# Performance work log

Hardware: AMD Instinct MI355X
Metric: run time of the kernel (lower is better)

The kernel has to match this reference:

```python
import jax, jax.numpy as jnp
import numpy as np

B, N, A, IN_DIM, OUT_DIM, D_OBS = 4096, 16, 8, 128, 128, 128


def setup_inputs() -> dict:
    key = jax.random.key(0)
    k1, k2, k3, k4, k5, k6 = jax.random.split(key, 6)
    h = jax.random.normal(k1, (B, N, IN_DIM), dtype=jnp.float32)
    policies = jax.random.uniform(k2, (B, N, A), dtype=jnp.float32)
    actions = jax.random.uniform(k3, (B, N, A), dtype=jnp.float32)
    obs_proc = jax.random.normal(k4, (B * N, D_OBS), dtype=jnp.float32)
    # xavier-normal-ish params (exact init values irrelevant for correctness baseline)
    W_fc = jax.random.normal(k5, (OUT_DIM, IN_DIM), dtype=jnp.float32) * (2.0 / (IN_DIM + OUT_DIM)) ** 0.5
    W_attn = jax.random.normal(k6, (1, 2 * OUT_DIM), dtype=jnp.float32) * (2.0 / (2 * OUT_DIM + 1)) ** 0.5
    return {"h": h, "policies": policies, "actions": actions, "obs_proc": obs_proc,
            "W_fc": W_fc, "W_attn": W_attn}


def reference(h, policies, actions, obs_proc, W_fc, W_attn):
    # h: [B, N, in_dim]; policies/actions: [B, N, A]; obs_proc: [B*N, D]
    b, n, a = policies.shape
    z = jnp.einsum('bni,oi->bno', h, W_fc)                    # fc(h), [B, N, out]
    out_dim = z.shape[-1]
    # attn_fc(cat[z_src, z_dst]) split into src/dst contributions
    a_src = z @ W_attn[0, :out_dim]                           # [B, N]
    a_dst = z @ W_attn[0, out_dim:]                           # [B, N]
    # e[b, i(dst), j(src)] = leaky_relu(a_src[b,j] + a_dst[b,i])
    e = jax.nn.leaky_relu(a_src[:, None, :] + a_dst[:, :, None], 0.01)
    w = jax.nn.sigmoid(e)[..., None]                          # [B, N(dst), N(src), 1]
    # gated mix of source action / source policy per (dst, src) pair
    zgate = w * actions[:, None, :, :] + (1.0 - w) * policies[:, None, :, :]  # [B,i,j,A]
    # repeat + place_policies/place_zs masked sum + mean over src dim collapses to:
    # out_z[b,i,k] = (sum_j zgate[b,i,j] - zgate[b,i,k] + policies[b,k]) / N
    sum_z = zgate.sum(axis=2)                                 # [B, i, A]
    out_z = (sum_z[:, :, None, :] - zgate + policies[:, None, :, :]) / n  # [B,i,k,A]
    obs_b = obs_proc.reshape(b, n, -1)                        # [B, k, D]
    d = obs_b.shape[-1]
    obs_rep = jnp.broadcast_to(obs_b[:, None, :, :], (b, n, n, d))  # [B, i, k, D]
    obs_final = jnp.concatenate([obs_rep, out_z], axis=-1).reshape(b * n, n, d + a)
    return obs_final, w.reshape(b * n, n, 1)
```

## Files before the change

kernel.cpp:

```cpp
#include <hip/hip_runtime.h>
#include <math.h>

#define B_SZ 4096
#define N_SZ 16
#define A_SZ 8
#define IN_DIM 128
#define OUT_DIM 128
#define D_OBS 128
#define ROW_OUT (D_OBS + A_SZ)

typedef float f32x4 __attribute__((ext_vector_type(4)));

__global__ __launch_bounds__(256) void prep_v(const float* __restrict__ W_fc,
                                              const float* __restrict__ W_attn,
                                              float* __restrict__ v) {
  __shared__ float part[2][2][128];
  const int i = threadIdx.x & 127;
  const int half = threadIdx.x >> 7;
  float s = 0.f, d = 0.f;
  #pragma unroll 8
  for (int oo = 0; oo < 64; ++oo) {
    const int o = half * 64 + oo;
    const float w = W_fc[o * IN_DIM + i];
    s += w * W_attn[o];
    d += w * W_attn[OUT_DIM + o];
  }
  part[half][0][i] = s;
  part[half][1][i] = d;
  __syncthreads();
  if (half == 0) {
    v[i]          = part[0][0][i] + part[1][0][i];
    v[IN_DIM + i] = part[0][1][i] + part[1][1][i];
  }
}

__global__ __launch_bounds__(256) void gat_main(
    const float* __restrict__ h,
    const float* __restrict__ pol,
    const float* __restrict__ act,
    const float* __restrict__ obs,
    const float* __restrict__ v,
    float* __restrict__ out_obs,
    float* __restrict__ out_w)
{
  const int b = blockIdx.x;
  const int tid = threadIdx.x;

  __shared__ float a_src_sm[16];
  __shared__ float a_dst_sm[16];
  __shared__ float w_sm[256];
  __shared__ float pol_sm[128];
  __shared__ float act_sm[128];
  __shared__ float sumz_sm[128];
  __shared__ float outz_sm[2048];
  __shared__ float obs_sm[2048];

  {
    const f32x4* op = (const f32x4*)(obs + (size_t)b * (N_SZ * D_OBS));
    f32x4* od = (f32x4*)obs_sm;
    od[tid]       = __builtin_nontemporal_load(&op[tid]);
    od[tid + 256] = __builtin_nontemporal_load(&op[tid + 256]);
  }
  if (tid < 128) {
    pol_sm[tid] = __builtin_nontemporal_load(&pol[(size_t)b * (N_SZ * A_SZ) + tid]);
    act_sm[tid] = __builtin_nontemporal_load(&act[(size_t)b * (N_SZ * A_SZ) + tid]);
  }

  {
    const int n = tid >> 4;
    const int l = tid & 15;
    const f32x4* hp = (const f32x4*)(h + (size_t)b * (N_SZ * IN_DIM));
    const f32x4 h0 = __builtin_nontemporal_load(&hp[tid * 2]);
    const f32x4 h1 = __builtin_nontemporal_load(&hp[tid * 2 + 1]);
    const f32x4* vs = (const f32x4*)v;
    const f32x4* vd = (const f32x4*)(v + IN_DIM);
    const f32x4 s0 = vs[l * 2], s1 = vs[l * 2 + 1];
    const f32x4 d0 = vd[l * 2], d1 = vd[l * 2 + 1];
    float s = h0.x * s0.x + h0.y * s0.y + h0.z * s0.z + h0.w * s0.w
            + h1.x * s1.x + h1.y * s1.y + h1.z * s1.z + h1.w * s1.w;
    float d = h0.x * d0.x + h0.y * d0.y + h0.z * d0.z + h0.w * d0.w
            + h1.x * d1.x + h1.y * d1.y + h1.z * d1.z + h1.w * d1.w;
    for (int m = 8; m >= 1; m >>= 1) {
      s += __shfl_xor(s, m, 16);
      d += __shfl_xor(d, m, 16);
    }
    if (l == 0) {
      a_src_sm[n] = s;
      a_dst_sm[n] = d;
    }
  }
  __syncthreads();

  {
    const int i = tid >> 4, j = tid & 15;
    float e = a_src_sm[j] + a_dst_sm[i];
    e = (e >= 0.f) ? e : 0.01f * e;
    const float wv = 1.f / (1.f + expf(-e));
    w_sm[tid] = wv;
    __builtin_nontemporal_store(wv, &out_w[(size_t)b * 256 + tid]);
  }
  __syncthreads();

  if (tid < 128) {
    const int i = tid >> 3, a = tid & 7;
    float s = 0.f;
    for (int j = 0; j < N_SZ; ++j) {
      const float wv = w_sm[i * 16 + j];
      s += wv * act_sm[j * 8 + a] + (1.f - wv) * pol_sm[j * 8 + a];
    }
    sumz_sm[tid] = s;
  }
  __syncthreads();

  {
    const int i = tid >> 4, k = tid & 15;
    const float wv = w_sm[tid];
    for (int a = 0; a < A_SZ; ++a) {
      const float zg = wv * act_sm[k * 8 + a] + (1.f - wv) * pol_sm[k * 8 + a];
      outz_sm[tid * 8 + a] =
          (sumz_sm[i * 8 + a] - zg + pol_sm[k * 8 + a]) * 0.0625f;
    }
  }
  __syncthreads();

  float* ob = out_obs + (size_t)b * (256 * ROW_OUT);
  const f32x4* obs4 = (const f32x4*)obs_sm;
  #pragma unroll 2
  for (int idx = tid; idx < 256 * 34; idx += 256) {
    const int r = idx / 34;
    const int d4 = idx - r * 34;
    f32x4 o4;
    if (d4 < 32) {
      const int k = r & 15;
      o4 = obs4[k * 32 + d4];
    } else {
      o4 = *(const f32x4*)(outz_sm + r * 8 + (d4 - 32) * 4);
    }
    __builtin_nontemporal_store(o4, (f32x4*)(ob + (size_t)idx * 4));
  }
}

extern "C" void kernel_launch(void* const* d_in, const int* in_sizes, int n_in,
                              void* d_out, int out_size, void* d_ws, size_t ws_size,
                              hipStream_t stream) {
  const float* h      = (const float*)d_in[0];
  const float* pol    = (const float*)d_in[1];
  const float* act    = (const float*)d_in[2];
  const float* obs    = (const float*)d_in[3];
  const float* W_fc   = (const float*)d_in[4];
  const float* W_attn = (const float*)d_in[5];

  float* out = (float*)d_out;
  float* out_w = out + (size_t)B_SZ * N_SZ * N_SZ * ROW_OUT;
  float* v = (float*)d_ws;

  prep_v<<<1, 256, 0, stream>>>(W_fc, W_attn, v);
  gat_main<<<B_SZ, 256, 0, stream>>>(h, pol, act, obs, v, out, out_w);
}
```

Before: 138.8 us.

## Split obs broadcast into separate grid-stride streaming kernel, widen prep reduction

The monolithic per-batch kernel is split in two. One kernel computes the attention weights and writes the 8-float gate columns of each output row directly from registers. A separate grid-stride kernel copies the broadcast obs rows into the first 128 columns of each output row. The prep kernel also uses 1024 threads with 8 partial sums instead of 256. This removes the large shared-memory staging and per-block syncs, and the copy loop drops its branch. In exchange it adds a third launch and leaves two kernels writing interleaved parts of the same rows, so each row's 544-byte span is covered by two partial, strided writes.

```diff
diff --git a/kernel.cpp b/kernel.cpp
--- a/kernel.cpp
+++ b/kernel.cpp
@@ -11,34 +11,36 @@
 
 typedef float f32x4 __attribute__((ext_vector_type(4)));
 
-__global__ __launch_bounds__(256) void prep_v(const float* __restrict__ W_fc,
-                                              const float* __restrict__ W_attn,
-                                              float* __restrict__ v) {
-  __shared__ float part[2][2][128];
+__global__ __launch_bounds__(1024) void prep_v(const float* __restrict__ W_fc,
+                                               const float* __restrict__ W_attn,
+                                               float* __restrict__ v) {
+  __shared__ float part[8][2][128];
   const int i = threadIdx.x & 127;
-  const int half = threadIdx.x >> 7;
+  const int seg = threadIdx.x >> 7;
   float s = 0.f, d = 0.f;
-  #pragma unroll 8
-  for (int oo = 0; oo < 64; ++oo) {
-    const int o = half * 64 + oo;
+  #pragma unroll
+  for (int oo = 0; oo < 16; ++oo) {
+    const int o = seg * 16 + oo;
     const float w = W_fc[o * IN_DIM + i];
     s += w * W_attn[o];
     d += w * W_attn[OUT_DIM + o];
   }
-  part[half][0][i] = s;
-  part[half][1][i] = d;
+  part[seg][0][i] = s;
+  part[seg][1][i] = d;
   __syncthreads();
-  if (half == 0) {
-    v[i]          = part[0][0][i] + part[1][0][i];
-    v[IN_DIM + i] = part[0][1][i] + part[1][1][i];
+  if (seg == 0) {
+    float ss = 0.f, dd = 0.f;
+    #pragma unroll
+    for (int t = 0; t < 8; ++t) { ss += part[t][0][i]; dd += part[t][1][i]; }
+    v[i] = ss;
+    v[IN_DIM + i] = dd;
   }
 }
 
-__global__ __launch_bounds__(256) void gat_main(
+__global__ __launch_bounds__(256) void gat_compute(
     const float* __restrict__ h,
     const float* __restrict__ pol,
     const float* __restrict__ act,
-    const float* __restrict__ obs,
     const float* __restrict__ v,
     float* __restrict__ out_obs,
     float* __restrict__ out_w)
@@ -52,15 +54,7 @@
   __shared__ float pol_sm[128];
   __shared__ float act_sm[128];
   __shared__ float sumz_sm[128];
-  __shared__ float outz_sm[2048];
-  __shared__ float obs_sm[2048];
 
-  {
-    const f32x4* op = (const f32x4*)(obs + (size_t)b * (N_SZ * D_OBS));
-    f32x4* od = (f32x4*)obs_sm;
-    od[tid]       = __builtin_nontemporal_load(&op[tid]);
-    od[tid + 256] = __builtin_nontemporal_load(&op[tid + 256]);
-  }
   if (tid < 128) {
     pol_sm[tid] = __builtin_nontemporal_load(&pol[(size_t)b * (N_SZ * A_SZ) + tid]);
     act_sm[tid] = __builtin_nontemporal_load(&act[(size_t)b * (N_SZ * A_SZ) + tid]);
@@ -113,30 +107,37 @@
   __syncthreads();
 
   {
-    const int i = tid >> 4, k = tid & 15;
+    const int k = tid & 15;
     const float wv = w_sm[tid];
+    float o8[8];
+    #pragma unroll
     for (int a = 0; a < A_SZ; ++a) {
       const float zg = wv * act_sm[k * 8 + a] + (1.f - wv) * pol_sm[k * 8 + a];
-      outz_sm[tid * 8 + a] =
-          (sumz_sm[i * 8 + a] - zg + pol_sm[k * 8 + a]) * 0.0625f;
+      o8[a] = (sumz_sm[(tid >> 4) * 8 + a] - zg + pol_sm[k * 8 + a]) * 0.0625f;
     }
+    const size_t row = (size_t)b * 256 + tid;
+    f32x4* dst = (f32x4*)(out_obs + row * ROW_OUT + D_OBS);
+    f32x4 lo = {o8[0], o8[1], o8[2], o8[3]};
+    f32x4 hi = {o8[4], o8[5], o8[6], o8[7]};
+    __builtin_nontemporal_store(lo, dst);
+    __builtin_nontemporal_store(hi, dst + 1);
   }
-  __syncthreads();
+}
 
-  float* ob = out_obs + (size_t)b * (256 * ROW_OUT);
-  const f32x4* obs4 = (const f32x4*)obs_sm;
-  #pragma unroll 2
-  for (int idx = tid; idx < 256 * 34; idx += 256) {
-    const int r = idx / 34;
-    const int d4 = idx - r * 34;
-    f32x4 o4;
-    if (d4 < 32) {
-      const int k = r & 15;
-      o4 = obs4[k * 32 + d4];
-    } else {
-      o4 = *(const f32x4*)(outz_sm + r * 8 + (d4 - 32) * 4);
-    }
-    __builtin_nontemporal_store(o4, (f32x4*)(ob + (size_t)idx * 4));
+__global__ __launch_bounds__(256) void gat_stream(
+    const float* __restrict__ obs,
+    float* __restrict__ out_obs)
+{
+  const f32x4* __restrict__ obs4 = (const f32x4*)obs;
+  const size_t total = (size_t)B_SZ * 256 * 32;
+  const size_t stride = (size_t)gridDim.x * blockDim.x;
+  for (size_t idx = (size_t)blockIdx.x * blockDim.x + threadIdx.x;
+       idx < total; idx += stride) {
+    const int q  = (int)(idx >> 5);
+    const int d4 = (int)(idx & 31);
+    const int bk = ((q >> 8) << 4) | (q & 15);
+    const f32x4 o = obs4[(size_t)bk * 32 + d4];
+    __builtin_nontemporal_store(o, (f32x4*)(out_obs) + (size_t)q * 34 + d4);
   }
 }
 
@@ -154,6 +155,7 @@
   float* out_w = out + (size_t)B_SZ * N_SZ * N_SZ * ROW_OUT;
   float* v = (float*)d_ws;
 
-  prep_v<<<1, 256, 0, stream>>>(W_fc, W_attn, v);
-  gat_main<<<B_SZ, 256, 0, stream>>>(h, pol, act, obs, v, out, out_w);
+  prep_v<<<1, 1024, 0, stream>>>(W_fc, W_attn, v);
+  gat_compute<<<B_SZ, 256, 0, stream>>>(h, pol, act, v, out, out_w);
+  gat_stream<<<2048, 256, 0, stream>>>(obs, out);
 }
```

Result: slower. 275.6 us (+98.6%).
